# Performance work log

Measured on AMD Instinct MI355X. Metric: run time of the kernel, lower is better.

## Reference

```python
import jax, jax.numpy as jnp
import numpy as np

B, H, S, D = 4, 16, 2048, 128

def setup_inputs() -> dict:
    key = jax.random.key(0)
    kq, kk, kv = jax.random.split(key, 3)
    Q = jax.random.normal(kq, (B, H, S, D), dtype=jnp.float32)
    K = jax.random.normal(kk, (B, H, S, D), dtype=jnp.float32)
    V = jax.random.normal(kv, (B, H, S, D), dtype=jnp.float32)
    # causal mask: True = attend (lower triangle incl. diagonal)
    mask = jnp.tril(jnp.ones((S, S), dtype=jnp.bool_))[None, None, :, :]
    return {"Q": Q, "K": K, "V": V, "mask": mask}

def reference(Q, K, V, mask):
    d_k = Q.shape[-1]
    scale = 1.0 / jnp.sqrt(jnp.asarray(d_k, Q.dtype))
    # [B,H,Sq,Sk] score matrix (naive, materialized, as in the original)
    scores = jnp.einsum('bhqd,bhkd->bhqk', Q, K) * scale
    scores = jnp.where(mask, scores, jnp.asarray(-1e9, scores.dtype))
    attn = jax.nn.softmax(scores, axis=-1)
    return jnp.einsum('bhqk,bhkd->bhqd', attn, V)
```

## Files before the change

kernel.cpp:

```cpp
#include <hip/hip_runtime.h>
#include <hip/hip_bf16.h>

constexpr int S_LEN = 2048;
constexpr int D_DIM = 128;
constexpr int NBH   = 64;
constexpr int NKT   = 32;
constexpr size_t TILE_SHORTS = 64 * 128;
constexpr size_t PAIR_SHORTS = 2 * TILE_SHORTS;
constexpr size_t WS_NEEDED   = (size_t)NBH * NKT * PAIR_SHORTS * 2;

typedef __attribute__((ext_vector_type(8))) short short8;
typedef __attribute__((ext_vector_type(4))) float f32x4;

__device__ __forceinline__ short f2bf(float f) {
    unsigned u = __builtin_bit_cast(unsigned, f);
    u += 0x7fffu + ((u >> 16) & 1u);
    return (short)(u >> 16);
}

__device__ __forceinline__ int kpos(int dc, int key) { return dc ^ (key & 15); }
__device__ __forceinline__ int vpos(int kc, int d) {
    return kc ^ ((d >> 3) & 7) ^ (d & 7);
}

__global__ __launch_bounds__(256)
void preprocess_kv(const float* __restrict__ K, const float* __restrict__ V,
                   short* __restrict__ ws) {
    __shared__ short sv[128 * 64];
    const int tid = threadIdx.x;
    const int kt  = blockIdx.x;
    const int bh  = blockIdx.y;
    const size_t inbase = ((size_t)bh * S_LEN + (size_t)kt * 64) * D_DIM;
    short* wk = ws + ((size_t)bh * NKT + kt) * PAIR_SHORTS;
    short* wv = wk + TILE_SHORTS;

    for (int it = 0; it < 4; ++it) {
        const int idx = (it * 256 + tid) * 8;
        const int key = idx >> 7, d = idx & 127;
        const float* kp = K + inbase + (size_t)key * D_DIM + d;
        float4 a = *reinterpret_cast<const float4*>(kp);
        float4 b = *reinterpret_cast<const float4*>(kp + 4);
        short8 f;
        f[0]=f2bf(a.x); f[1]=f2bf(a.y); f[2]=f2bf(a.z); f[3]=f2bf(a.w);
        f[4]=f2bf(b.x); f[5]=f2bf(b.y); f[6]=f2bf(b.z); f[7]=f2bf(b.w);
        *reinterpret_cast<short8*>(&wk[key * 128 + (kpos(d >> 3, key) << 3)]) = f;
        const float* vp = V + inbase + (size_t)key * D_DIM + d;
        float4 c = *reinterpret_cast<const float4*>(vp);
        float4 e = *reinterpret_cast<const float4*>(vp + 4);
        float vals[8] = {c.x,c.y,c.z,c.w,e.x,e.y,e.z,e.w};
        for (int j = 0; j < 8; ++j) {
            const int dr = d + j;
            sv[dr * 64 + (vpos(key >> 3, dr) << 3) + (key & 7)] = f2bf(vals[j]);
        }
    }
    __syncthreads();
    for (int it = 0; it < 4; ++it) {
        const int off = (it * 256 + tid) * 8;
        *reinterpret_cast<short8*>(&wv[off]) =
            *reinterpret_cast<const short8*>(&sv[off]);
    }
}

__device__ __forceinline__ void async_copy_1k(const short* gsrc, short* ldst,
                                              int lane) {
    __builtin_amdgcn_global_load_lds(
        (const __attribute__((address_space(1))) void*)(gsrc + lane * 8),
        (__attribute__((address_space(3))) void*)ldst, 16, 0, 0);
}
__device__ __forceinline__ void dma_tile16k(const short* gsrc, short* ldst,
                                            int wid, int lane) {
    for (int i = 0; i < 4; ++i) {
        const int s = wid * 4 + i;
        async_copy_1k(gsrc + s * 512, ldst + s * 512, lane);
    }
}

__global__ __launch_bounds__(256, 4)
void fa_causal_main(const float* __restrict__ Q, const short* __restrict__ ws,
                    float* __restrict__ Out) {
    __shared__ short sK [64 * 128];
    __shared__ short sVt[128 * 64];
    __shared__ short sP [64 * 64];

    const int tid  = threadIdx.x;
    const int wid  = tid >> 6;
    const int lane = tid & 63;
    const int quad = lane >> 4;
    const int l16  = lane & 15;

    const int x  = blockIdx.x;
    const int bh = blockIdx.y;
    const size_t base = (size_t)bh * S_LEN * D_DIM;
    const short* tiles = ws + (size_t)bh * NKT * PAIR_SHORTS;
    const float scale = 0.08838834764831845f;

    for (int pi = 0; pi < 2; ++pi) {
        const int qt = (pi == 0) ? (31 - x) : x;
        const int q0 = qt * 64;

        short8 q_frag[4];
        {
            const float* qp = Q + base + (size_t)(q0 + wid * 16 + l16) * D_DIM;
            for (int kk = 0; kk < 4; ++kk) {
                const int d0 = kk * 32 + quad * 8;
                float4 a = *reinterpret_cast<const float4*>(qp + d0);
                float4 b = *reinterpret_cast<const float4*>(qp + d0 + 4);
                short8 f;
                f[0]=f2bf(a.x*scale); f[1]=f2bf(a.y*scale);
                f[2]=f2bf(a.z*scale); f[3]=f2bf(a.w*scale);
                f[4]=f2bf(b.x*scale); f[5]=f2bf(b.y*scale);
                f[6]=f2bf(b.z*scale); f[7]=f2bf(b.w*scale);
                q_frag[kk] = f;
            }
        }

        f32x4 o_acc[8];
        for (int i = 0; i < 8; ++i) o_acc[i] = f32x4{0.f,0.f,0.f,0.f};
        float m_i[4], l_i[4];
        for (int r = 0; r < 4; ++r) { m_i[r] = -1e30f; l_i[r] = 0.f; }

        dma_tile16k(tiles, sK, wid, lane);
        dma_tile16k(tiles + TILE_SHORTS, sVt, wid, lane);

        for (int kt = 0; kt <= qt; ++kt) {
            __syncthreads();

            f32x4 s_acc[4];
            for (int ct = 0; ct < 4; ++ct) {
                const int key = ct * 16 + l16;
                f32x4 acc = f32x4{0.f,0.f,0.f,0.f};
                for (int kk = 0; kk < 4; ++kk) {
                    short8 kf = *reinterpret_cast<const short8*>(
                        &sK[key * 128 + (kpos(kk * 4 + quad, key) << 3)]);
                    acc = __builtin_amdgcn_mfma_f32_16x16x32_bf16(q_frag[kk], kf, acc, 0, 0, 0);
                }
                s_acc[ct] = acc;
            }

            if (kt == qt) {
                for (int ct = 0; ct < 4; ++ct) {
                    const int kg = ct * 16 + l16;
                    for (int r = 0; r < 4; ++r)
                        if (kg > wid * 16 + quad * 4 + r) s_acc[ct][r] = -1e30f;
                }
            }

            float tm[4];
            for (int r = 0; r < 4; ++r)
                tm[r] = fmaxf(fmaxf(s_acc[0][r], s_acc[1][r]),
                              fmaxf(s_acc[2][r], s_acc[3][r]));
            for (int off = 1; off < 16; off <<= 1)
                for (int r = 0; r < 4; ++r)
                    tm[r] = fmaxf(tm[r], __shfl_xor(tm[r], off));
            float alpha[4], m_new[4], rs[4];
            for (int r = 0; r < 4; ++r) {
                m_new[r] = fmaxf(m_i[r], tm[r]);
                alpha[r] = __expf(m_i[r] - m_new[r]);
                rs[r] = 0.f;
            }
            for (int ct = 0; ct < 4; ++ct)
                for (int r = 0; r < 4; ++r) {
                    float p = __expf(s_acc[ct][r] - m_new[r]);
                    s_acc[ct][r] = p;
                    rs[r] += p;
                }
            for (int off = 1; off < 16; off <<= 1)
                for (int r = 0; r < 4; ++r)
                    rs[r] += __shfl_xor(rs[r], off);
            for (int r = 0; r < 4; ++r) {
                l_i[r] = alpha[r] * l_i[r] + rs[r];
                m_i[r] = m_new[r];
            }
            for (int nt = 0; nt < 8; ++nt)
                for (int r = 0; r < 4; ++r)
                    o_acc[nt][r] *= alpha[r];

            __syncthreads();

            if (kt < qt)
                dma_tile16k(tiles + (size_t)(kt + 1) * PAIR_SHORTS, sK, wid, lane);

            for (int ct = 0; ct < 4; ++ct)
                for (int r = 0; r < 4; ++r) {
                    const int row = wid * 16 + quad * 4 + r;
                    const int col = ct * 16 + l16;
                    sP[row * 64 + (((col >> 3) ^ (row & 7)) << 3) + (col & 7)]
                        = f2bf(s_acc[ct][r]);
                }

            {
                const int prow = wid * 16 + l16;
                short8 pf[2];
                for (int k2 = 0; k2 < 2; ++k2)
                    pf[k2] = *reinterpret_cast<const short8*>(
                        &sP[prow * 64 + (((k2 * 4 + quad) ^ (prow & 7)) << 3)]);
                for (int nt = 0; nt < 8; ++nt) {
                    const int vrow = nt * 16 + l16;
                    for (int k2 = 0; k2 < 2; ++k2) {
                        short8 vf = *reinterpret_cast<const short8*>(
                            &sVt[vrow * 64 + (vpos(k2 * 4 + quad, vrow) << 3)]);
                        o_acc[nt] = __builtin_amdgcn_mfma_f32_16x16x32_bf16(pf[k2], vf, o_acc[nt], 0, 0, 0);
                    }
                }
            }

            __syncthreads();

            if (kt < qt)
                dma_tile16k(tiles + (size_t)(kt + 1) * PAIR_SHORTS + TILE_SHORTS,
                            sVt, wid, lane);
        }

        for (int nt = 0; nt < 8; ++nt)
            for (int r = 0; r < 4; ++r) {
                const int qrow = q0 + wid * 16 + quad * 4 + r;
                Out[base + (size_t)qrow * D_DIM + nt * 16 + l16] = o_acc[nt][r] / l_i[r];
            }
    }
}

constexpr int SK_STRIDE  = 136;
constexpr int SVT_STRIDE = 72;
constexpr int SP_STRIDE  = 72;

__global__ __launch_bounds__(256, 4)
void fa_causal_fallback(const float* __restrict__ Q, const float* __restrict__ K,
                        const float* __restrict__ V, float* __restrict__ Out) {
    __shared__ short sK[64 * SK_STRIDE];
    __shared__ short sVt[128 * SVT_STRIDE];
    short* sP = sK;
    const int tid  = threadIdx.x;
    const int wid  = tid >> 6;
    const int lane = tid & 63;
    const int quad = lane >> 4;
    const int l16  = lane & 15;
    const int x  = blockIdx.x;
    const int bh = blockIdx.y;
    const size_t base = (size_t)bh * S_LEN * D_DIM;
    const float scale = 0.08838834764831845f;
    for (int pi = 0; pi < 2; ++pi) {
        const int qt = (pi == 0) ? (31 - x) : x;
        const int q0 = qt * 64;
        short8 q_frag[4];
        {
            const float* qp = Q + base + (size_t)(q0 + wid * 16 + l16) * D_DIM;
            for (int kk = 0; kk < 4; ++kk) {
                const int d0 = kk * 32 + quad * 8;
                float4 a = *reinterpret_cast<const float4*>(qp + d0);
                float4 b = *reinterpret_cast<const float4*>(qp + d0 + 4);
                short8 f;
                f[0]=f2bf(a.x*scale); f[1]=f2bf(a.y*scale);
                f[2]=f2bf(a.z*scale); f[3]=f2bf(a.w*scale);
                f[4]=f2bf(b.x*scale); f[5]=f2bf(b.y*scale);
                f[6]=f2bf(b.z*scale); f[7]=f2bf(b.w*scale);
                q_frag[kk] = f;
            }
        }
        f32x4 o_acc[8];
        for (int i = 0; i < 8; ++i) o_acc[i] = f32x4{0.f,0.f,0.f,0.f};
        float m_i[4], l_i[4];
        for (int r = 0; r < 4; ++r) { m_i[r] = -1e30f; l_i[r] = 0.f; }
        for (int kt = 0; kt <= qt; ++kt) {
            for (int it = 0; it < 4; ++it) {
                const int idx = (it * 256 + tid) * 8;
                const int key = idx >> 7, d = idx & 127;
                const float* kp = K + base + (size_t)(kt * 64 + key) * D_DIM + d;
                float4 a = *reinterpret_cast<const float4*>(kp);
                float4 b = *reinterpret_cast<const float4*>(kp + 4);
                short8 f;
                f[0]=f2bf(a.x); f[1]=f2bf(a.y); f[2]=f2bf(a.z); f[3]=f2bf(a.w);
                f[4]=f2bf(b.x); f[5]=f2bf(b.y); f[6]=f2bf(b.z); f[7]=f2bf(b.w);
                *reinterpret_cast<short8*>(&sK[key * SK_STRIDE + d]) = f;
            }
            for (int it = 0; it < 4; ++it) {
                const int idx = (it * 256 + tid) * 8;
                const int key = idx >> 7, d = idx & 127;
                const int kc = key >> 3, kw = key & 7;
                const float* vp = V + base + (size_t)(kt * 64 + key) * D_DIM + d;
                float4 a = *reinterpret_cast<const float4*>(vp);
                float4 b = *reinterpret_cast<const float4*>(vp + 4);
                float vals[8] = {a.x,a.y,a.z,a.w,b.x,b.y,b.z,b.w};
                const int rc = (d >> 3) & 7;
                const int cs = (kc ^ rc) * 8 + kw;
                for (int j = 0; j < 8; ++j)
                    sVt[(d + j) * SVT_STRIDE + cs] = f2bf(vals[j]);
            }
            __syncthreads();
            f32x4 s_acc[4];
            for (int ct = 0; ct < 4; ++ct) {
                f32x4 acc = f32x4{0.f,0.f,0.f,0.f};
                for (int kk = 0; kk < 4; ++kk) {
                    short8 kf = *reinterpret_cast<const short8*>(
                        &sK[(ct * 16 + l16) * SK_STRIDE + kk * 32 + quad * 8]);
                    acc = __builtin_amdgcn_mfma_f32_16x16x32_bf16(q_frag[kk], kf, acc, 0, 0, 0);
                }
                s_acc[ct] = acc;
            }
            if (kt == qt) {
                for (int ct = 0; ct < 4; ++ct) {
                    const int kg = ct * 16 + l16;
                    for (int r = 0; r < 4; ++r)
                        if (kg > wid * 16 + quad * 4 + r) s_acc[ct][r] = -1e30f;
                }
            }
            float tm[4];
            for (int r = 0; r < 4; ++r)
                tm[r] = fmaxf(fmaxf(s_acc[0][r], s_acc[1][r]),
                              fmaxf(s_acc[2][r], s_acc[3][r]));
            for (int off = 1; off < 16; off <<= 1)
                for (int r = 0; r < 4; ++r)
                    tm[r] = fmaxf(tm[r], __shfl_xor(tm[r], off));
            float alpha[4], m_new[4], rs[4];
            for (int r = 0; r < 4; ++r) {
                m_new[r] = fmaxf(m_i[r], tm[r]);
                alpha[r] = __expf(m_i[r] - m_new[r]);
                rs[r] = 0.f;
            }
            for (int ct = 0; ct < 4; ++ct)
                for (int r = 0; r < 4; ++r) {
                    float p = __expf(s_acc[ct][r] - m_new[r]);
                    s_acc[ct][r] = p;
                    rs[r] += p;
                }
            for (int off = 1; off < 16; off <<= 1)
                for (int r = 0; r < 4; ++r)
                    rs[r] += __shfl_xor(rs[r], off);
            for (int r = 0; r < 4; ++r) {
                l_i[r] = alpha[r] * l_i[r] + rs[r];
                m_i[r] = m_new[r];
            }
            for (int nt = 0; nt < 8; ++nt)
                for (int r = 0; r < 4; ++r)
                    o_acc[nt][r] *= alpha[r];
            __syncthreads();
            for (int ct = 0; ct < 4; ++ct)
                for (int r = 0; r < 4; ++r) {
                    const int row = wid * 16 + quad * 4 + r;
                    const int col = ct * 16 + l16;
                    sP[row * SP_STRIDE + (((col >> 3) ^ ((row >> 2) & 7)) << 3) + (col & 7)]
                        = f2bf(s_acc[ct][r]);
                }
            {
                const int prow = wid * 16 + l16;
                const int pxr  = (prow >> 2) & 7;
                for (int nt = 0; nt < 8; ++nt) {
                    const int vrow = nt * 16 + l16;
                    const int vxr  = (vrow >> 3) & 7;
                    for (int k2 = 0; k2 < 2; ++k2) {
                        const int chunk = k2 * 4 + quad;
                        short8 pf = *reinterpret_cast<const short8*>(
                            &sP[prow * SP_STRIDE + ((chunk ^ pxr) << 3)]);
                        short8 vf = *reinterpret_cast<const short8*>(
                            &sVt[vrow * SVT_STRIDE + ((chunk ^ vxr) << 3)]);
                        o_acc[nt] = __builtin_amdgcn_mfma_f32_16x16x32_bf16(pf, vf, o_acc[nt], 0, 0, 0);
                    }
                }
            }
            __syncthreads();
        }
        for (int nt = 0; nt < 8; ++nt)
            for (int r = 0; r < 4; ++r) {
                const int qrow = q0 + wid * 16 + quad * 4 + r;
                Out[base + (size_t)qrow * D_DIM + nt * 16 + l16] = o_acc[nt][r] / l_i[r];
            }
    }
}

extern "C" void kernel_launch(void* const* d_in, const int* in_sizes, int n_in,
                              void* d_out, int out_size, void* d_ws, size_t ws_size,
                              hipStream_t stream) {
    const float* Q = (const float*)d_in[0];
    const float* K = (const float*)d_in[1];
    const float* V = (const float*)d_in[2];
    float* Out = (float*)d_out;

    if (ws_size >= WS_NEEDED) {
        short* ws = (short*)d_ws;
        preprocess_kv<<<dim3(NKT, NBH), 256, 0, stream>>>(K, V, ws);
        fa_causal_main<<<dim3(16, NBH), 256, 0, stream>>>(Q, ws, Out);
    } else {
        fa_causal_fallback<<<dim3(16, NBH), 256, 0, stream>>>(Q, K, V, Out);
    }
}
```

Baseline: 432.8 us.

## Use 128-row query tiles, double-buffered K, register-staged V, lazy rescaling

The main kernel now runs 512-thread blocks that each handle 128 query rows, so every K/V tile loaded into shared memory serves twice as many queries. K is double-buffered with async global-to-LDS copies and the next V tile is prefetched into registers, which removes one barrier per iteration and the load stall. Softmax moves to exp2 with log2e folded into the Q scale, rescales only when the running max grows by more than 8, raises wave priority around the MFMA sections, and lets warps whose rows are fully masked skip work. The block-to-tile mapping is also reordered. The costs are more registers and LDS per block, and idle waves in the diagonal tiles.

```diff
diff --git a/kernel.cpp b/kernel.cpp
--- a/kernel.cpp
+++ b/kernel.cpp
@@ -67,20 +67,13 @@
         (const __attribute__((address_space(1))) void*)(gsrc + lane * 8),
         (__attribute__((address_space(3))) void*)ldst, 16, 0, 0);
 }
-__device__ __forceinline__ void dma_tile16k(const short* gsrc, short* ldst,
-                                            int wid, int lane) {
-    for (int i = 0; i < 4; ++i) {
-        const int s = wid * 4 + i;
-        async_copy_1k(gsrc + s * 512, ldst + s * 512, lane);
-    }
-}
-
-__global__ __launch_bounds__(256, 4)
+
+__global__ __launch_bounds__(512, 4)
 void fa_causal_main(const float* __restrict__ Q, const short* __restrict__ ws,
                     float* __restrict__ Out) {
-    __shared__ short sK [64 * 128];
+    __shared__ short sK[2][64 * 128];
     __shared__ short sVt[128 * 64];
-    __shared__ short sP [64 * 64];
+    __shared__ short sP [128 * 64];
 
     const int tid  = threadIdx.x;
     const int wid  = tid >> 6;
@@ -88,15 +81,31 @@
     const int quad = lane >> 4;
     const int l16  = lane & 15;
 
-    const int x  = blockIdx.x;
-    const int bh = blockIdx.y;
+    const int k_ = blockIdx.x;
+    const int j_ = blockIdx.y;
+    const int bh = k_ * 8 + (j_ >> 3);
+    const int x  = j_ & 7;
+
     const size_t base = (size_t)bh * S_LEN * D_DIM;
     const short* tiles = ws + (size_t)bh * NKT * PAIR_SHORTS;
-    const float scale = 0.08838834764831845f;
-
+    const float qscale = 0.08838834764831845f * 1.44269504088896340f;
+
+    int nb = 0;
     for (int pi = 0; pi < 2; ++pi) {
-        const int qt = (pi == 0) ? (31 - x) : x;
-        const int q0 = qt * 64;
+        const int qt = (pi == 0) ? (15 - x) : x;
+        const int q0 = qt * 128;
+        const int kend = 2 * qt + 2;
+
+        for (int i = 0; i < 2; ++i) {
+            const int s = wid * 2 + i;
+            async_copy_1k(tiles + s * 512, &sK[nb][s * 512], lane);
+        }
+        short8 vr0, vr1;
+        {
+            const short* vp = tiles + TILE_SHORTS;
+            vr0 = *reinterpret_cast<const short8*>(vp + tid * 8);
+            vr1 = *reinterpret_cast<const short8*>(vp + tid * 8 + 4096);
+        }
 
         short8 q_frag[4];
         {
@@ -106,10 +115,10 @@
                 float4 a = *reinterpret_cast<const float4*>(qp + d0);
                 float4 b = *reinterpret_cast<const float4*>(qp + d0 + 4);
                 short8 f;
-                f[0]=f2bf(a.x*scale); f[1]=f2bf(a.y*scale);
-                f[2]=f2bf(a.z*scale); f[3]=f2bf(a.w*scale);
-                f[4]=f2bf(b.x*scale); f[5]=f2bf(b.y*scale);
-                f[6]=f2bf(b.z*scale); f[7]=f2bf(b.w*scale);
+                f[0]=f2bf(a.x*qscale); f[1]=f2bf(a.y*qscale);
+                f[2]=f2bf(a.z*qscale); f[3]=f2bf(a.w*qscale);
+                f[4]=f2bf(b.x*qscale); f[5]=f2bf(b.y*qscale);
+                f[6]=f2bf(b.z*qscale); f[7]=f2bf(b.w*qscale);
                 q_frag[kk] = f;
             }
         }
@@ -119,81 +128,101 @@
         float m_i[4], l_i[4];
         for (int r = 0; r < 4; ++r) { m_i[r] = -1e30f; l_i[r] = 0.f; }
 
-        dma_tile16k(tiles, sK, wid, lane);
-        dma_tile16k(tiles + TILE_SHORTS, sVt, wid, lane);
-
-        for (int kt = 0; kt <= qt; ++kt) {
+        for (int kt = 0; kt < kend; ++kt) {
             __syncthreads();
 
+            *reinterpret_cast<short8*>(&sVt[tid * 8]) = vr0;
+            *reinterpret_cast<short8*>(&sVt[tid * 8 + 4096]) = vr1;
+
+            if (kt + 1 < kend) {
+                const short* nk = tiles + (size_t)(kt + 1) * PAIR_SHORTS;
+                for (int i = 0; i < 2; ++i) {
+                    const int s = wid * 2 + i;
+                    async_copy_1k(nk + s * 512, &sK[nb ^ 1][s * 512], lane);
+                }
+                const short* nv = nk + TILE_SHORTS;
+                vr0 = *reinterpret_cast<const short8*>(nv + tid * 8);
+                vr1 = *reinterpret_cast<const short8*>(nv + tid * 8 + 4096);
+            }
+
+            const int kb    = kt * 64;
+            const int wrow0 = q0 + wid * 16;
+            const bool active = (kb <= wrow0 + 15);
+
             f32x4 s_acc[4];
-            for (int ct = 0; ct < 4; ++ct) {
-                const int key = ct * 16 + l16;
-                f32x4 acc = f32x4{0.f,0.f,0.f,0.f};
-                for (int kk = 0; kk < 4; ++kk) {
-                    short8 kf = *reinterpret_cast<const short8*>(
-                        &sK[key * 128 + (kpos(kk * 4 + quad, key) << 3)]);
-                    acc = __builtin_amdgcn_mfma_f32_16x16x32_bf16(q_frag[kk], kf, acc, 0, 0, 0);
-                }
-                s_acc[ct] = acc;
-            }
-
-            if (kt == qt) {
+            if (active) {
+                __builtin_amdgcn_s_setprio(1);
                 for (int ct = 0; ct < 4; ++ct) {
-                    const int kg = ct * 16 + l16;
+                    const int key = ct * 16 + l16;
+                    f32x4 acc = f32x4{0.f,0.f,0.f,0.f};
+                    for (int kk = 0; kk < 4; ++kk) {
+                        short8 kf = *reinterpret_cast<const short8*>(
+                            &sK[nb][key * 128 + (kpos(kk * 4 + quad, key) << 3)]);
+                        acc = __builtin_amdgcn_mfma_f32_16x16x32_bf16(q_frag[kk], kf, acc, 0, 0, 0);
+                    }
+                    s_acc[ct] = acc;
+                }
+                __builtin_amdgcn_s_setprio(0);
+
+                if (kb + 63 > wrow0) {
+                    for (int ct = 0; ct < 4; ++ct) {
+                        const int kg = kb + ct * 16 + l16;
+                        for (int r = 0; r < 4; ++r)
+                            if (kg > wrow0 + quad * 4 + r) s_acc[ct][r] = -1e30f;
+                    }
+                }
+
+                float tm[4];
+                for (int r = 0; r < 4; ++r)
+                    tm[r] = fmaxf(fmaxf(s_acc[0][r], s_acc[1][r]),
+                                  fmaxf(s_acc[2][r], s_acc[3][r]));
+                for (int off = 1; off < 16; off <<= 1)
                     for (int r = 0; r < 4; ++r)
-                        if (kg > wid * 16 + quad * 4 + r) s_acc[ct][r] = -1e30f;
-                }
-            }
-
-            float tm[4];
-            for (int r = 0; r < 4; ++r)
-                tm[r] = fmaxf(fmaxf(s_acc[0][r], s_acc[1][r]),
-                              fmaxf(s_acc[2][r], s_acc[3][r]));
-            for (int off = 1; off < 16; off <<= 1)
+                        tm[r] = fmaxf(tm[r], __shfl_xor(tm[r], off));
+                bool grow = false;
                 for (int r = 0; r < 4; ++r)
-                    tm[r] = fmaxf(tm[r], __shfl_xor(tm[r], off));
-            float alpha[4], m_new[4], rs[4];
-            for (int r = 0; r < 4; ++r) {
-                m_new[r] = fmaxf(m_i[r], tm[r]);
-                alpha[r] = __expf(m_i[r] - m_new[r]);
-                rs[r] = 0.f;
-            }
-            for (int ct = 0; ct < 4; ++ct)
-                for (int r = 0; r < 4; ++r) {
-                    float p = __expf(s_acc[ct][r] - m_new[r]);
-                    s_acc[ct][r] = p;
-                    rs[r] += p;
-                }
-            for (int off = 1; off < 16; off <<= 1)
-                for (int r = 0; r < 4; ++r)
-                    rs[r] += __shfl_xor(rs[r], off);
-            for (int r = 0; r < 4; ++r) {
-                l_i[r] = alpha[r] * l_i[r] + rs[r];
-                m_i[r] = m_new[r];
-            }
-            for (int nt = 0; nt < 8; ++nt)
-                for (int r = 0; r < 4; ++r)
-                    o_acc[nt][r] *= alpha[r];
-
-            __syncthreads();
-
-            if (kt < qt)
-                dma_tile16k(tiles + (size_t)(kt + 1) * PAIR_SHORTS, sK, wid, lane);
-
-            for (int ct = 0; ct < 4; ++ct)
-                for (int r = 0; r < 4; ++r) {
-                    const int row = wid * 16 + quad * 4 + r;
-                    const int col = ct * 16 + l16;
-                    sP[row * 64 + (((col >> 3) ^ (row & 7)) << 3) + (col & 7)]
-                        = f2bf(s_acc[ct][r]);
-                }
-
-            {
+                    grow = grow || (tm[r] - m_i[r] > 8.0f);
+                if (__any(grow)) {
+                    for (int r = 0; r < 4; ++r) {
+                        const float mn = fmaxf(m_i[r], tm[r]);
+                        const float a  = __builtin_amdgcn_exp2f(m_i[r] - mn);
+                        m_i[r] = mn;
+                        l_i[r] *= a;
+                        for (int nt = 0; nt < 8; ++nt) o_acc[nt][r] *= a;
+                    }
+                }
+                float rs[4] = {0.f, 0.f, 0.f, 0.f};
+                for (int ct = 0; ct < 4; ++ct)
+                    for (int r = 0; r < 4; ++r) {
+                        const float p = __builtin_amdgcn_exp2f(s_acc[ct][r] - m_i[r]);
+                        s_acc[ct][r] = p;
+                        rs[r] += p;
+                    }
+                for (int off = 1; off < 16; off <<= 1)
+                    for (int r = 0; r < 4; ++r)
+                        rs[r] += __shfl_xor(rs[r], off);
+                for (int r = 0; r < 4; ++r) l_i[r] += rs[r];
+
+                for (int ct = 0; ct < 4; ++ct)
+                    for (int r = 0; r < 4; ++r) {
+                        const int row = wid * 16 + quad * 4 + r;
+                        const int col = ct * 16 + l16;
+                        sP[row * 64 + (((col >> 3) ^ (row & 7)) << 3) + (col & 7)]
+                            = f2bf(s_acc[ct][r]);
+                    }
+            }
+
+            asm volatile("s_waitcnt lgkmcnt(0)" ::: "memory");
+            __builtin_amdgcn_s_barrier();
+            asm volatile("" ::: "memory");
+
+            if (active) {
                 const int prow = wid * 16 + l16;
                 short8 pf[2];
                 for (int k2 = 0; k2 < 2; ++k2)
                     pf[k2] = *reinterpret_cast<const short8*>(
                         &sP[prow * 64 + (((k2 * 4 + quad) ^ (prow & 7)) << 3)]);
+                __builtin_amdgcn_s_setprio(1);
                 for (int nt = 0; nt < 8; ++nt) {
                     const int vrow = nt * 16 + l16;
                     for (int k2 = 0; k2 < 2; ++k2) {
@@ -202,20 +231,18 @@
                         o_acc[nt] = __builtin_amdgcn_mfma_f32_16x16x32_bf16(pf[k2], vf, o_acc[nt], 0, 0, 0);
                     }
                 }
-            }
-
-            __syncthreads();
-
-            if (kt < qt)
-                dma_tile16k(tiles + (size_t)(kt + 1) * PAIR_SHORTS + TILE_SHORTS,
-                            sVt, wid, lane);
-        }
-
-        for (int nt = 0; nt < 8; ++nt)
-            for (int r = 0; r < 4; ++r) {
-                const int qrow = q0 + wid * 16 + quad * 4 + r;
-                Out[base + (size_t)qrow * D_DIM + nt * 16 + l16] = o_acc[nt][r] / l_i[r];
-            }
+                __builtin_amdgcn_s_setprio(0);
+            }
+            nb ^= 1;
+        }
+
+        for (int r = 0; r < 4; ++r) {
+            const float inv = 1.0f / l_i[r];
+            const int qrow = q0 + wid * 16 + quad * 4 + r;
+            float* op = Out + base + (size_t)qrow * D_DIM;
+            for (int nt = 0; nt < 8; ++nt)
+                op[nt * 16 + l16] = o_acc[nt][r] * inv;
+        }
     }
 }
 
@@ -377,7 +404,7 @@
     if (ws_size >= WS_NEEDED) {
         short* ws = (short*)d_ws;
         preprocess_kv<<<dim3(NKT, NBH), 256, 0, stream>>>(K, V, ws);
-        fa_causal_main<<<dim3(16, NBH), 256, 0, stream>>>(Q, ws, Out);
+        fa_causal_main<<<dim3(8, NBH), 512, 0, stream>>>(Q, ws, Out);
     } else {
         fa_causal_fallback<<<dim3(16, NBH), 256, 0, stream>>>(Q, K, V, Out);
     }
```

After: 465.8 us. 7.6% more time.
